# Kernel optimization log

Hardware: AMD Instinct MI355X
Metric: run time of the kernel (lower is better)

Reference implementation:

```python
import jax, jax.numpy as jnp
import numpy as np

N_NODES = 50000
N_EDGES = 800000
NUM_GRAPHS = 256
F_IN = 64        # num_features (per-head out dim == in dim in this module)
HEADS = 4        # n_heads1
OUT_DIM = 128    # output_dim
HC = HEADS * F_IN
NEG_SLOPE = 0.2  # GATConv leaky_relu slope
EPS = 1e-5       # GraphNorm eps


def setup_inputs() -> dict:
    key = jax.random.key(0)
    ks = jax.random.split(key, 12)
    s = lambda k, shape, fan: (jax.random.normal(k, shape, jnp.float32) / np.sqrt(fan).astype(np.float32))
    return {
        "x": jax.random.normal(ks[0], (N_NODES, F_IN), jnp.float32),
        "edge_index": jax.random.randint(ks[1], (2, N_EDGES), 0, N_NODES),
        "batch": jnp.sort(jax.random.randint(ks[2], (N_NODES,), 0, NUM_GRAPHS)),
        # GATConv params
        "lin_w": s(ks[3], (HC, F_IN), F_IN),
        "att_src": s(ks[4], (HEADS, F_IN), F_IN),
        "att_dst": s(ks[5], (HEADS, F_IN), F_IN),
        "gat_bias": jnp.zeros((HC,), jnp.float32),
        # GraphNorm params
        "gn_weight": jnp.ones((HC,), jnp.float32),
        "gn_bias": jnp.zeros((HC,), jnp.float32),
        "gn_mean_scale": jnp.ones((HC,), jnp.float32),
        # fc_g1 / out heads
        "fc1_w": s(ks[6], (OUT_DIM, HC), HC), "fc1_b": jnp.zeros((OUT_DIM,), jnp.float32),
        "out_w": s(ks[7], (1, OUT_DIM), OUT_DIM), "out_b": jnp.zeros((1,), jnp.float32),
        # GlobalAttention gate_nn: Linear(HC,16) -> ReLU -> Linear(16,1) -> Sigmoid
        "att1_w": s(ks[8], (16, HC), HC), "att1_b": jnp.zeros((16,), jnp.float32),
        "att2_w": s(ks[9], (1, 16), 16), "att2_b": jnp.zeros((1,), jnp.float32),
    }


def _gat_conv(x, edge_index, lin_w, att_src, att_dst, gat_bias):
    """PyG GATConv with add_self_loops=True, concat heads. Returns (out [N,HC], alpha [E+N,H])."""
    N = x.shape[0]
    xh = (x @ lin_w.T).reshape(N, HEADS, F_IN)                 # [N,H,C]
    a_src = (xh * att_src[None]).sum(-1)                        # [N,H]
    a_dst = (xh * att_dst[None]).sum(-1)                        # [N,H]
    loops = jnp.arange(N)
    src = jnp.concatenate([edge_index[0], loops])               # [E+N]
    dst = jnp.concatenate([edge_index[1], loops])
    alpha = jax.nn.leaky_relu(a_src[src] + a_dst[dst], NEG_SLOPE)  # [E+N,H]
    # segment softmax over incoming edges of each dst node (self-loops guarantee non-empty)
    amax = jax.ops.segment_max(alpha, dst, num_segments=N)
    alpha = jnp.exp(alpha - amax[dst])
    denom = jax.ops.segment_sum(alpha, dst, num_segments=N)
    alpha = alpha / (denom[dst] + 1e-16)
    msg = xh[src] * alpha[:, :, None]                           # [E+N,H,C]
    out = jax.ops.segment_sum(msg, dst, num_segments=N).reshape(N, HC) + gat_bias
    return out, alpha


def _graph_norm(x, batch, weight, bias, mean_scale):
    ones = jnp.ones((x.shape[0],), x.dtype)
    cnt = jnp.maximum(jax.ops.segment_sum(ones, batch, num_segments=NUM_GRAPHS), 1.0)[:, None]
    mean = jax.ops.segment_sum(x, batch, num_segments=NUM_GRAPHS) / cnt
    sub = x - mean[batch] * mean_scale
    var = jax.ops.segment_sum(sub * sub, batch, num_segments=NUM_GRAPHS) / cnt
    return weight * sub / jnp.sqrt(var + EPS)[batch] + bias


def _global_attention(x, batch, att1_w, att1_b, att2_w, att2_b):
    gate = jax.nn.sigmoid(jax.nn.relu(x @ att1_w.T + att1_b) @ att2_w.T + att2_b)  # [N,1]
    gmax = jax.ops.segment_max(gate, batch, num_segments=NUM_GRAPHS)
    gate = jnp.exp(gate - gmax[batch])
    gden = jax.ops.segment_sum(gate, batch, num_segments=NUM_GRAPHS)
    gate = gate / (gden[batch] + 1e-16)
    return jax.ops.segment_sum(gate * x, batch, num_segments=NUM_GRAPHS)  # [G,HC]


def reference(x, edge_index, batch, lin_w, att_src, att_dst, gat_bias,
              gn_weight, gn_bias, gn_mean_scale, fc1_w, fc1_b, out_w, out_b,
              att1_w, att1_b, att2_w, att2_b):
    x2, alpha = _gat_conv(x, edge_index, lin_w, att_src, att_dst, gat_bias)
    h = _graph_norm(x2, batch, gn_weight, gn_bias, gn_mean_scale)
    h = jax.nn.relu(h)                                # node_dropout = identity (eval)
    pooled = _global_attention(h, batch, att1_w, att1_b, att2_w, att2_b)
    h = jax.nn.relu(pooled @ fc1_w.T + fc1_b)          # dropout = identity (eval)
    out = jax.nn.sigmoid(h @ out_w.T + out_b)          # [G,1]
    return out, alpha
```

## Files before the change

kernel.cpp:

```cpp
#include <hip/hip_runtime.h>
#include <hip/hip_fp16.h>
#include <math.h>

#define NN 50000
#define NE 800000
#define NG 256
#define NEG_SLOPE 0.2f
#define GEPS 1e-5f
#define CHUNK 64
#define NB 196
#define CAP 6144
#define EPB 3125
#define SPLIT 8
#define NLINB 782
#define ABLK 3321

typedef _Float16 f16x8 __attribute__((ext_vector_type(8)));
typedef _Float16 f16x4 __attribute__((ext_vector_type(4)));
typedef float f32x4 __attribute__((ext_vector_type(4)));
typedef float f32x2 __attribute__((ext_vector_type(2)));

__device__ __forceinline__ float lrelu(float v){ return v > 0.f ? v : NEG_SLOPE * v; }

__global__ __launch_bounds__(256) void k_misc(const float* __restrict__ lin_w,
                                              _Float16* __restrict__ wh,
                                              const float* __restrict__ att1_w,
                                              _Float16* __restrict__ a1w,
                                              const int* __restrict__ batch,
                                              int* __restrict__ goff,
                                              int* __restrict__ gcnt,
                                              int* __restrict__ bucket_cnt) {
  int b = blockIdx.x, tid = threadIdx.x;
  if (b == 0) {
    if (tid < NB) bucket_cnt[tid] = 0;
    int g = tid;
    int lo = 0, hi = NN;
    while (lo < hi) { int mid = (lo + hi) >> 1; if (batch[mid] < g) lo = mid + 1; else hi = mid; }
    int start = lo;
    lo = 0; hi = NN;
    while (lo < hi) { int mid = (lo + hi) >> 1; if (batch[mid] < g + 1) lo = mid + 1; else hi = mid; }
    goff[g] = start;
    gcnt[g] = lo - start;
  } else if (b <= 16) {
    int i0 = (b - 1) * 1024 + tid * 4;
    float4 f = *(const float4*)&lin_w[i0];
    f16x4 h4;
    h4[0] = (_Float16)f.x; h4[1] = (_Float16)f.y; h4[2] = (_Float16)f.z; h4[3] = (_Float16)f.w;
    *(f16x4*)&wh[i0] = h4;
  } else {
    int i0 = (b - 17) * 1024 + tid * 4;
    float4 f = *(const float4*)&att1_w[i0];
    f16x4 h4;
    h4[0] = (_Float16)f.x; h4[1] = (_Float16)f.y; h4[2] = (_Float16)f.z; h4[3] = (_Float16)f.w;
    *(f16x4*)&a1w[i0] = h4;
  }
}

__device__ __forceinline__ void lin_body(char* smem,
                                         const float* __restrict__ x,
                                         const _Float16* __restrict__ wh,
                                         const float* __restrict__ att_src,
                                         const float* __restrict__ att_dst,
                                         unsigned char* __restrict__ xh8,
                                         float* __restrict__ a_src_n,
                                         float* __restrict__ a_dst_n) {
  unsigned char* s_f8 = (unsigned char*)smem;
  int w = threadIdx.x >> 6, lane = threadIdx.x & 63;
  int nb = blockIdx.x * 64 + w * 16;
  if (nb >= NN) return;
  int am = lane & 15, quad = lane >> 4;
  int wb = w * 4096;

  const float* xr = x + (size_t)(nb + am) * 64 + quad * 8;
  float4 f0 = *(const float4*)(xr);
  float4 f1 = *(const float4*)(xr + 4);
  float4 f2 = *(const float4*)(xr + 32);
  float4 f3 = *(const float4*)(xr + 36);
  f16x8 a0, a1;
  a0[0] = (_Float16)f0.x; a0[1] = (_Float16)f0.y; a0[2] = (_Float16)f0.z; a0[3] = (_Float16)f0.w;
  a0[4] = (_Float16)f1.x; a0[5] = (_Float16)f1.y; a0[6] = (_Float16)f1.z; a0[7] = (_Float16)f1.w;
  a1[0] = (_Float16)f2.x; a1[1] = (_Float16)f2.y; a1[2] = (_Float16)f2.z; a1[3] = (_Float16)f2.w;
  a1[4] = (_Float16)f3.x; a1[5] = (_Float16)f3.y; a1[6] = (_Float16)f3.z; a1[7] = (_Float16)f3.w;

  f32x4 acc[16];
#pragma unroll
  for (int ct = 0; ct < 16; ct++) acc[ct] = (f32x4){0.f, 0.f, 0.f, 0.f};

#pragma unroll
  for (int ct = 0; ct < 16; ct++) {
    const _Float16* wbp = wh + (size_t)(ct * 16 + am) * 64 + quad * 8;
    f16x8 b0 = *(const f16x8*)(wbp);
    f16x8 b1 = *(const f16x8*)(wbp + 32);
    acc[ct] = __builtin_amdgcn_mfma_f32_16x16x32_f16(a0, b0, acc[ct], 0, 0, 0);
    acc[ct] = __builtin_amdgcn_mfma_f32_16x16x32_f16(a1, b1, acc[ct], 0, 0, 0);
  }

  float ps[4][4], pd[4][4];
#pragma unroll
  for (int r = 0; r < 4; r++)
#pragma unroll
    for (int h = 0; h < 4; h++) { ps[r][h] = 0.f; pd[r][h] = 0.f; }
#pragma unroll
  for (int ct = 0; ct < 16; ct++) {
    int c = ct * 16 + am;
    float av = att_src[c];
    float dv = att_dst[c];
    int h = ct >> 2;
#pragma unroll
    for (int r = 0; r < 4; r++) {
      float v = acc[ct][r];
      ps[r][h] += v * av;
      pd[r][h] += v * dv;
    }
  }
#pragma unroll
  for (int r = 0; r < 4; r++)
#pragma unroll
    for (int h = 0; h < 4; h++) {
      float s = ps[r][h], d = pd[r][h];
#pragma unroll
      for (int o = 1; o < 16; o <<= 1) {
        s += __shfl_xor(s, o, 64);
        d += __shfl_xor(d, o, 64);
      }
      if (am == 0) {
        int node = nb + quad * 4 + r;
        a_src_n[node * 4 + h] = s;
        a_dst_n[node * 4 + h] = d;
      }
    }

#pragma unroll
  for (int r = 0; r < 4; r++) {
    uint4 u;
    int t;
    t = __builtin_amdgcn_cvt_pk_fp8_f32(acc[0][r],  acc[1][r],  0, 0);
    t = __builtin_amdgcn_cvt_pk_fp8_f32(acc[2][r],  acc[3][r],  t, 1);
    u.x = (unsigned)t;
    t = __builtin_amdgcn_cvt_pk_fp8_f32(acc[4][r],  acc[5][r],  0, 0);
    t = __builtin_amdgcn_cvt_pk_fp8_f32(acc[6][r],  acc[7][r],  t, 1);
    u.y = (unsigned)t;
    t = __builtin_amdgcn_cvt_pk_fp8_f32(acc[8][r],  acc[9][r],  0, 0);
    t = __builtin_amdgcn_cvt_pk_fp8_f32(acc[10][r], acc[11][r], t, 1);
    u.z = (unsigned)t;
    t = __builtin_amdgcn_cvt_pk_fp8_f32(acc[12][r], acc[13][r], 0, 0);
    t = __builtin_amdgcn_cvt_pk_fp8_f32(acc[14][r], acc[15][r], t, 1);
    u.w = (unsigned)t;
    *(uint4*)&s_f8[wb + (quad * 4 + r) * 256 + am * 16] = u;
  }
#pragma unroll
  for (int p = 0; p < 4; p++) {
    uint4 u = *(const uint4*)&s_f8[wb + p * 1024 + lane * 16];
    *(uint4*)&xh8[(size_t)nb * 256 + p * 1024 + lane * 16] = u;
  }
}

__device__ __forceinline__ void binA_body(char* smem, int b,
                                          const int* __restrict__ ei,
                                          int* __restrict__ bucket_cnt,
                                          int2* __restrict__ ebuf) {
  int2* sorted = (int2*)smem;
  int*  hist   = (int*)(smem + 25024);
  int*  lbase  = (int*)(smem + 25824);
  int*  cur    = (int*)(smem + 26624);
  int*  runb   = (int*)(smem + 27424);
  int*  wsum   = (int*)(smem + 28224);
  int tid = threadIdx.x, lane = tid & 63, wid = tid >> 6;
  int e0 = b * EPB, e1 = min(e0 + EPB, NE);
  int n = e1 - e0;
  for (int i = tid; i < NB; i += 256) hist[i] = 0;
  __syncthreads();
  for (int e = e0 + tid; e < e1; e += 256) atomicAdd(&hist[ei[NE + e] >> 8], 1);
  __syncthreads();
  {
    int v = (tid < NB) ? hist[tid] : 0;
    int s = v;
#pragma unroll
    for (int o = 1; o < 64; o <<= 1) { int t = __shfl_up(s, o, 64); if (lane >= o) s += t; }
    if (lane == 63) wsum[wid] = s;
    __syncthreads();
    int wbase = 0;
    for (int k = 0; k < wid; k++) wbase += wsum[k];
    if (tid < NB) {
      int ex = wbase + s - v;
      lbase[tid] = ex;
      cur[tid] = ex;
      runb[tid] = atomicAdd(&bucket_cnt[tid], v);
    }
  }
  __syncthreads();
  for (int e = e0 + tid; e < e1; e += 256) {
    int d = ei[NE + e], s = ei[e];
    int lp = atomicAdd(&cur[d >> 8], 1);
    sorted[lp] = make_int2(d, s);
  }
  __syncthreads();
  for (int i = tid; i < n; i += 256) {
    int2 e = sorted[i];
    int bk = e.x >> 8;
    int slot = runb[bk] + (i - lbase[bk]);
    if (slot < CAP) ebuf[(size_t)bk * CAP + slot] = e;
  }
}

__global__ __launch_bounds__(256) void k_linbin(const float* __restrict__ x,
                                                const _Float16* __restrict__ wh,
                                                const float* __restrict__ att_src,
                                                const float* __restrict__ att_dst,
                                                unsigned char* __restrict__ xh8,
                                                float* __restrict__ a_src_n,
                                                float* __restrict__ a_dst_n,
                                                const int* __restrict__ ei,
                                                int* __restrict__ bucket_cnt,
                                                int2* __restrict__ ebuf) {
  __shared__ __align__(16) char smem[28240];
  if (blockIdx.x < NLINB)
    lin_body(smem, x, wh, att_src, att_dst, xh8, a_src_n, a_dst_n);
  else
    binA_body(smem, blockIdx.x - NLINB, ei, bucket_cnt, ebuf);
}

__global__ __launch_bounds__(256) void k_binB(const int2* __restrict__ ebuf,
                                              const int* __restrict__ bucket_cnt,
                                              int* __restrict__ deg,
                                              int* __restrict__ offs,
                                              int* __restrict__ src_list) {
  __shared__ int hist[256];
  __shared__ int cur[256];
  __shared__ int wsum[4];
  __shared__ int bbase[NB];
  int b = blockIdx.x, tid = threadIdx.x, lane = tid & 63, wid = tid >> 6;
  {
    int v = (tid < NB) ? min(bucket_cnt[tid], CAP) : 0;
    int s = v;
#pragma unroll
    for (int o = 1; o < 64; o <<= 1) { int t = __shfl_up(s, o, 64); if (lane >= o) s += t; }
    if (lane == 63) wsum[wid] = s;
    __syncthreads();
    int wbase = 0;
    for (int k = 0; k < wid; k++) wbase += wsum[k];
    if (tid < NB) bbase[tid] = wbase + s - v;
  }
  __syncthreads();
  int cnt = min(bucket_cnt[b], CAP);
  int base = bbase[b];
  const int2* seg = ebuf + (size_t)b * CAP;
  hist[tid] = 0;
  __syncthreads();
  for (int i = tid; i < cnt; i += 256) atomicAdd(&hist[seg[i].x & 255], 1);
  __syncthreads();
  int v = hist[tid];
  int s = v;
#pragma unroll
  for (int o = 1; o < 64; o <<= 1) { int t = __shfl_up(s, o, 64); if (lane >= o) s += t; }
  if (lane == 63) wsum[wid] = s;
  __syncthreads();
  int wbase = 0;
  for (int k = 0; k < wid; k++) wbase += wsum[k];
  int excl = wbase + s - v;
  int node = b * 256 + tid;
  if (node < NN) {
    deg[node] = v;
    offs[node] = base + excl;
  }
  cur[tid] = excl;
  __syncthreads();
  for (int i = tid; i < cnt; i += 256) {
    int2 e = seg[i];
    int pos = base + atomicAdd(&cur[e.x & 255], 1);
    src_list[pos] = e.y;
  }
}

__global__ __launch_bounds__(64) void k_gat(const unsigned char* __restrict__ xh8,
                                            const float* __restrict__ a_src_n,
                                            const float* __restrict__ a_dst_n,
                                            const int* __restrict__ offs,
                                            const int* __restrict__ deg_arr,
                                            const int* __restrict__ src_list,
                                            const float* __restrict__ gat_bias,
                                            __half* __restrict__ x2h,
                                            float* __restrict__ den_inv) {
  __shared__ __align__(16) float s_al[CHUNK * 4];
  __shared__ int s_src[CHUNK];
  __shared__ __half s_tr[256];
  int n = blockIdx.x, lane = threadIdx.x;
  int off = offs[n], dg = deg_arr[n], cnt = dg + 1;
  float4 ad = *(const float4*)&a_dst_n[n * 4];
  int h = lane & 3;
  unsigned loff = 4u * (unsigned)lane;
  float acc0 = 0.f, acc1 = 0.f, acc2 = 0.f, acc3 = 0.f;

  if (cnt <= 64) {
    float e0 = 0.f, e1 = 0.f, e2 = 0.f, e3 = 0.f;
    if (lane < cnt) {
      int src = (lane < dg) ? src_list[off + lane] : n;
      float4 as = *(const float4*)&a_src_n[src * 4];
      e0 = __expf(lrelu(as.x + ad.x));
      e1 = __expf(lrelu(as.y + ad.y));
      e2 = __expf(lrelu(as.z + ad.z));
      e3 = __expf(lrelu(as.w + ad.w));
      s_src[lane] = src;
    }
    float s0 = e0, s1 = e1, s2 = e2, s3 = e3;
#pragma unroll
    for (int o = 32; o >= 1; o >>= 1) {
      s0 += __shfl_xor(s0, o, 64);
      s1 += __shfl_xor(s1, o, 64);
      s2 += __shfl_xor(s2, o, 64);
      s3 += __shfl_xor(s3, o, 64);
    }
    float i0 = 1.f / (s0 + 1e-16f), i1 = 1.f / (s1 + 1e-16f);
    float i2 = 1.f / (s2 + 1e-16f), i3 = 1.f / (s3 + 1e-16f);
    if (lane == 0) *(float4*)&den_inv[n * 4] = make_float4(i0, i1, i2, i3);
    if (lane < cnt) {
      s_al[lane * 4 + 0] = e0 * i0;
      s_al[lane * 4 + 1] = e1 * i1;
      s_al[lane * 4 + 2] = e2 * i2;
      s_al[lane * 4 + 3] = e3 * i3;
    }
    __syncthreads();
    int j = 0;
    for (; j + 4 <= cnt; j += 4) {
      unsigned oA = ((unsigned)s_src[j] << 8) + loff;
      unsigned oB = ((unsigned)s_src[j + 1] << 8) + loff;
      unsigned oC = ((unsigned)s_src[j + 2] << 8) + loff;
      unsigned oD = ((unsigned)s_src[j + 3] << 8) + loff;
      unsigned rA = *(const unsigned*)&xh8[oA];
      unsigned rB = *(const unsigned*)&xh8[oB];
      unsigned rC = *(const unsigned*)&xh8[oC];
      unsigned rD = *(const unsigned*)&xh8[oD];
      float aA = s_al[j * 4 + h], aB = s_al[(j + 1) * 4 + h];
      float aC = s_al[(j + 2) * 4 + h], aD = s_al[(j + 3) * 4 + h];
      f32x2 lA = __builtin_amdgcn_cvt_pk_f32_fp8((int)rA, 0);
      f32x2 hA = __builtin_amdgcn_cvt_pk_f32_fp8((int)rA, 1);
      f32x2 lB = __builtin_amdgcn_cvt_pk_f32_fp8((int)rB, 0);
      f32x2 hB = __builtin_amdgcn_cvt_pk_f32_fp8((int)rB, 1);
      f32x2 lC = __builtin_amdgcn_cvt_pk_f32_fp8((int)rC, 0);
      f32x2 hC = __builtin_amdgcn_cvt_pk_f32_fp8((int)rC, 1);
      f32x2 lD = __builtin_amdgcn_cvt_pk_f32_fp8((int)rD, 0);
      f32x2 hD = __builtin_amdgcn_cvt_pk_f32_fp8((int)rD, 1);
      acc0 += aA * lA[0] + aB * lB[0] + aC * lC[0] + aD * lD[0];
      acc1 += aA * lA[1] + aB * lB[1] + aC * lC[1] + aD * lD[1];
      acc2 += aA * hA[0] + aB * hB[0] + aC * hC[0] + aD * hD[0];
      acc3 += aA * hA[1] + aB * hB[1] + aC * hC[1] + aD * hD[1];
    }
    for (; j < cnt; j++) {
      unsigned oA = ((unsigned)s_src[j] << 8) + loff;
      unsigned rA = *(const unsigned*)&xh8[oA];
      float aA = s_al[j * 4 + h];
      f32x2 lA = __builtin_amdgcn_cvt_pk_f32_fp8((int)rA, 0);
      f32x2 hA = __builtin_amdgcn_cvt_pk_f32_fp8((int)rA, 1);
      acc0 += aA * lA[0];
      acc1 += aA * lA[1];
      acc2 += aA * hA[0];
      acc3 += aA * hA[1];
    }
  } else {
    float s0 = 0.f, s1 = 0.f, s2 = 0.f, s3 = 0.f;
    for (int j = lane; j < cnt; j += 64) {
      int src = (j < dg) ? src_list[off + j] : n;
      float4 as = *(const float4*)&a_src_n[src * 4];
      s0 += __expf(lrelu(as.x + ad.x));
      s1 += __expf(lrelu(as.y + ad.y));
      s2 += __expf(lrelu(as.z + ad.z));
      s3 += __expf(lrelu(as.w + ad.w));
    }
#pragma unroll
    for (int o = 32; o >= 1; o >>= 1) {
      s0 += __shfl_xor(s0, o, 64);
      s1 += __shfl_xor(s1, o, 64);
      s2 += __shfl_xor(s2, o, 64);
      s3 += __shfl_xor(s3, o, 64);
    }
    float i0 = 1.f / (s0 + 1e-16f), i1 = 1.f / (s1 + 1e-16f);
    float i2 = 1.f / (s2 + 1e-16f), i3 = 1.f / (s3 + 1e-16f);
    if (lane == 0) *(float4*)&den_inv[n * 4] = make_float4(i0, i1, i2, i3);
    for (int cb = 0; cb < cnt; cb += CHUNK) {
      int clen = min(CHUNK, cnt - cb);
      for (int j = lane; j < clen; j += 64) {
        int jj = cb + j;
        int src = (jj < dg) ? src_list[off + jj] : n;
        float4 as = *(const float4*)&a_src_n[src * 4];
        s_src[j] = src;
        s_al[j * 4 + 0] = __expf(lrelu(as.x + ad.x)) * i0;
        s_al[j * 4 + 1] = __expf(lrelu(as.y + ad.y)) * i1;
        s_al[j * 4 + 2] = __expf(lrelu(as.z + ad.z)) * i2;
        s_al[j * 4 + 3] = __expf(lrelu(as.w + ad.w)) * i3;
      }
      __syncthreads();
      for (int j = 0; j < clen; j++) {
        unsigned oA = ((unsigned)s_src[j] << 8) + loff;
        unsigned rA = *(const unsigned*)&xh8[oA];
        float aA = s_al[j * 4 + h];
        f32x2 lA = __builtin_amdgcn_cvt_pk_f32_fp8((int)rA, 0);
        f32x2 hA = __builtin_amdgcn_cvt_pk_f32_fp8((int)rA, 1);
        acc0 += aA * lA[0];
        acc1 += aA * lA[1];
        acc2 += aA * hA[0];
        acc3 += aA * hA[1];
      }
      __syncthreads();
    }
  }

  int cb0 = (lane & 3) * 64 + (lane >> 2);
  s_tr[cb0 +  0] = __float2half(acc0 + gat_bias[cb0 +  0]);
  s_tr[cb0 + 16] = __float2half(acc1 + gat_bias[cb0 + 16]);
  s_tr[cb0 + 32] = __float2half(acc2 + gat_bias[cb0 + 32]);
  s_tr[cb0 + 48] = __float2half(acc3 + gat_bias[cb0 + 48]);
  __syncthreads();
  uint2 u = *(const uint2*)&s_tr[4 * lane];
  *(uint2*)&x2h[(size_t)n * 256 + 4 * lane] = u;
}

__global__ __launch_bounds__(256) void k_alst(const int* __restrict__ ei,
                                              const float* __restrict__ a_src_n,
                                              const float* __restrict__ a_dst_n,
                                              const float* __restrict__ den_inv,
                                              float* __restrict__ alpha_out,
                                              const __half* __restrict__ x2h,
                                              const int* __restrict__ gcnt,
                                              const int* __restrict__ goff,
                                              float* __restrict__ psumA,
                                              float* __restrict__ psumB) {
  if (blockIdx.x < ABLK) {
    int idx = blockIdx.x * 256 + threadIdx.x;
    if (idx >= NE + NN) return;
    int s, d;
    if (idx < NE) { s = ei[idx]; d = ei[NE + idx]; }
    else          { s = idx - NE; d = s; }
    float4 as = *(const float4*)&a_src_n[s * 4];
    float4 ad = *(const float4*)&a_dst_n[d * 4];
    float4 iv = *(const float4*)&den_inv[d * 4];
    float4 a;
    a.x = __expf(lrelu(as.x + ad.x)) * iv.x;
    a.y = __expf(lrelu(as.y + ad.y)) * iv.y;
    a.z = __expf(lrelu(as.z + ad.z)) * iv.z;
    a.w = __expf(lrelu(as.w + ad.w)) * iv.w;
    *(float4*)&alpha_out[(size_t)idx * 4] = a;
  } else {
    int b = blockIdx.x - ABLK, c = threadIdx.x;
    int g = b >> 3, s = b & 7;
    int cnt = gcnt[g], start = goff[g];
    const __half* p = x2h + (size_t)start * 256 + c;
    float sum = 0.f, sum2 = 0.f;
    int i = s;
    for (; i + 56 < cnt; i += 64) {
      float v0 = __half2float(p[(size_t)(i +  0) * 256]);
      float v1 = __half2float(p[(size_t)(i +  8) * 256]);
      float v2 = __half2float(p[(size_t)(i + 16) * 256]);
      float v3 = __half2float(p[(size_t)(i + 24) * 256]);
      float v4 = __half2float(p[(size_t)(i + 32) * 256]);
      float v5 = __half2float(p[(size_t)(i + 40) * 256]);
      float v6 = __half2float(p[(size_t)(i + 48) * 256]);
      float v7 = __half2float(p[(size_t)(i + 56) * 256]);
      sum += ((v0 + v1) + (v2 + v3)) + ((v4 + v5) + (v6 + v7));
      sum2 += ((v0 * v0 + v1 * v1) + (v2 * v2 + v3 * v3)) +
              ((v4 * v4 + v5 * v5) + (v6 * v6 + v7 * v7));
    }
    for (; i < cnt; i += 8) { float v = __half2float(p[(size_t)i * 256]); sum += v; sum2 += v * v; }
    psumA[b * 256 + c] = sum;
    psumB[b * 256 + c] = sum2;
  }
}

__global__ __launch_bounds__(256) void k_stats2(const float* __restrict__ psumA,
                                                const float* __restrict__ psumB,
                                                const int* __restrict__ gcnt,
                                                const float* __restrict__ gn_w,
                                                const float* __restrict__ gn_b,
                                                const float* __restrict__ gn_ms,
                                                float* __restrict__ scale_g,
                                                float* __restrict__ shift_g) {
  int g = blockIdx.x, c = threadIdx.x;
  int b0 = g * SPLIT;
  float S = 0.f, S2 = 0.f;
#pragma unroll
  for (int k = 0; k < SPLIT; k++) {
    S  += psumA[(b0 + k) * 256 + c];
    S2 += psumB[(b0 + k) * 256 + c];
  }
  float fc = fmaxf((float)gcnt[g], 1.f);
  float mean = S / fc;
  float mm = mean * gn_ms[c];
  float var = fmaxf(S2 / fc - 2.f * mm * mean + mm * mm, 0.f);
  float sc = gn_w[c] / sqrtf(var + GEPS);
  scale_g[g * 256 + c] = sc;
  shift_g[g * 256 + c] = gn_b[c] - sc * mm;
}

__global__ __launch_bounds__(256) void k_gate(const __half* __restrict__ x2h,
                                              const int* __restrict__ batch,
                                              const float* __restrict__ scale_g,
                                              const float* __restrict__ shift_g,
                                              const _Float16* __restrict__ a1w,
                                              const float* __restrict__ att1_b,
                                              const float* __restrict__ att2_w,
                                              const float* __restrict__ att2_b,
                                              float* __restrict__ gate_raw) {
  int w = threadIdx.x >> 6, lane = threadIdx.x & 63;
  int nb = blockIdx.x * 64 + w * 16;
  if (nb >= NN) return;
  int am = lane & 15, quad = lane >> 4;
  int node = nb + am;
  int g = batch[node];

  const __half*   xp  = x2h + (size_t)node * 256 + quad * 8;
  const float*    scp = scale_g + g * 256 + quad * 8;
  const float*    shp = shift_g + g * 256 + quad * 8;
  const _Float16* bp  = a1w + am * 256 + quad * 8;

  f32x4 acc = (f32x4){0.f, 0.f, 0.f, 0.f};
#pragma unroll
  for (int kb = 0; kb < 8; kb++) {
    f16x8 xv = *(const f16x8*)(xp + kb * 32);
    float4 sc0 = *(const float4*)(scp + kb * 32);
    float4 sc1 = *(const float4*)(scp + kb * 32 + 4);
    float4 sh0 = *(const float4*)(shp + kb * 32);
    float4 sh1 = *(const float4*)(shp + kb * 32 + 4);
    f16x8 a;
    a[0] = (_Float16)fmaxf(sc0.x * (float)xv[0] + sh0.x, 0.f);
    a[1] = (_Float16)fmaxf(sc0.y * (float)xv[1] + sh0.y, 0.f);
    a[2] = (_Float16)fmaxf(sc0.z * (float)xv[2] + sh0.z, 0.f);
    a[3] = (_Float16)fmaxf(sc0.w * (float)xv[3] + sh0.w, 0.f);
    a[4] = (_Float16)fmaxf(sc1.x * (float)xv[4] + sh1.x, 0.f);
    a[5] = (_Float16)fmaxf(sc1.y * (float)xv[5] + sh1.y, 0.f);
    a[6] = (_Float16)fmaxf(sc1.z * (float)xv[6] + sh1.z, 0.f);
    a[7] = (_Float16)fmaxf(sc1.w * (float)xv[7] + sh1.w, 0.f);
    f16x8 b = *(const f16x8*)(bp + kb * 32);
    acc = __builtin_amdgcn_mfma_f32_16x16x32_f16(a, b, acc, 0, 0, 0);
  }

  float b1 = att1_b[am], w2 = att2_w[am], b2 = att2_b[0];
#pragma unroll
  for (int r = 0; r < 4; r++) {
    float t = w2 * fmaxf(acc[r] + b1, 0.f);
#pragma unroll
    for (int o = 1; o < 16; o <<= 1) t += __shfl_xor(t, o, 64);
    if (am == 0) gate_raw[nb + quad * 4 + r] = 1.f / (1.f + __expf(-(t + b2)));
  }
}

__global__ __launch_bounds__(256) void k_poolp(const __half* __restrict__ x2h,
                                               const float* __restrict__ gate_raw,
                                               const int* __restrict__ gcnt,
                                               const int* __restrict__ goff,
                                               const float* __restrict__ scale_g,
                                               const float* __restrict__ shift_g,
                                               float* __restrict__ ppool) {
  __shared__ float s_w[1024];
  __shared__ float red[4];
  int b = blockIdx.x, c = threadIdx.x, lane = c & 63, wid = c >> 6;
  int g = b >> 3, s = b & 7;
  int cnt = gcnt[g], start = goff[g];
  float ls = 0.f;
  for (int i = c; i < cnt; i += 256) {
    float e = __expf(gate_raw[start + i]);
    s_w[i] = e;
    ls += e;
  }
#pragma unroll
  for (int o = 32; o >= 1; o >>= 1) ls += __shfl_xor(ls, o, 64);
  if (lane == 0) red[wid] = ls;
  __syncthreads();
  float rden = 1.f / (red[0] + red[1] + red[2] + red[3] + 1e-16f);

  float sc = scale_g[g * 256 + c], sh = shift_g[g * 256 + c];
  const __half* p = x2h + (size_t)start * 256 + c;
  float pooled = 0.f;
  int i = s;
  for (; i + 56 < cnt; i += 64) {
    float v0 = __half2float(p[(size_t)(i +  0) * 256]);
    float v1 = __half2float(p[(size_t)(i +  8) * 256]);
    float v2 = __half2float(p[(size_t)(i + 16) * 256]);
    float v3 = __half2float(p[(size_t)(i + 24) * 256]);
    float v4 = __half2float(p[(size_t)(i + 32) * 256]);
    float v5 = __half2float(p[(size_t)(i + 40) * 256]);
    float v6 = __half2float(p[(size_t)(i + 48) * 256]);
    float v7 = __half2float(p[(size_t)(i + 56) * 256]);
    pooled += s_w[i +  0] * fmaxf(sc * v0 + sh, 0.f);
    pooled += s_w[i +  8] * fmaxf(sc * v1 + sh, 0.f);
    pooled += s_w[i + 16] * fmaxf(sc * v2 + sh, 0.f);
    pooled += s_w[i + 24] * fmaxf(sc * v3 + sh, 0.f);
    pooled += s_w[i + 32] * fmaxf(sc * v4 + sh, 0.f);
    pooled += s_w[i + 40] * fmaxf(sc * v5 + sh, 0.f);
    pooled += s_w[i + 48] * fmaxf(sc * v6 + sh, 0.f);
    pooled += s_w[i + 56] * fmaxf(sc * v7 + sh, 0.f);
  }
  for (; i < cnt; i += 8)
    pooled += s_w[i] * fmaxf(sc * __half2float(p[(size_t)i * 256]) + sh, 0.f);
  ppool[b * 256 + c] = pooled * rden;
}

__global__ __launch_bounds__(256) void k_fin(const float* __restrict__ ppool,
                                             const float* __restrict__ fc1_w,
                                             const float* __restrict__ fc1_b,
                                             const float* __restrict__ out_w,
                                             const float* __restrict__ out_b,
                                             float* __restrict__ outp) {
  __shared__ __align__(16) float pool_s[256];
  __shared__ float hred[128];
  __shared__ float red[4];
  int g = blockIdx.x, tid = threadIdx.x, lane = tid & 63, wid = tid >> 6;
  int b0 = g * SPLIT;
  float acc = 0.f;
#pragma unroll
  for (int k = 0; k < SPLIT; k++) acc += ppool[(b0 + k) * 256 + tid];
  pool_s[tid] = acc;
  __syncthreads();
  float4 psv = *(const float4*)&pool_s[4 * lane];
  for (int j0 = 0; j0 < 32; j0++) {
    int j = wid * 32 + j0;
    float4 w = *(const float4*)&fc1_w[j * 256 + 4 * lane];
    float d = w.x * psv.x + w.y * psv.y + w.z * psv.z + w.w * psv.w;
#pragma unroll
    for (int o = 32; o >= 1; o >>= 1) d += __shfl_xor(d, o, 64);
    if (lane == 0) hred[j] = fmaxf(d + fc1_b[j], 0.f) * out_w[j];
  }
  __syncthreads();
  if (tid < 128) {
    float v = hred[tid];
#pragma unroll
    for (int o = 32; o >= 1; o >>= 1) v += __shfl_xor(v, o, 64);
    if (lane == 0) red[wid] = v;
  }
  __syncthreads();
  if (tid == 0) outp[g] = 1.f / (1.f + __expf(-(red[0] + red[1] + out_b[0])));
}

extern "C" void kernel_launch(void* const* d_in, const int* in_sizes, int n_in,
                              void* d_out, int out_size, void* d_ws, size_t ws_size,
                              hipStream_t stream) {
  const float* x        = (const float*)d_in[0];
  const int*   ei       = (const int*)d_in[1];
  const int*   batch    = (const int*)d_in[2];
  const float* lin_w    = (const float*)d_in[3];
  const float* att_src  = (const float*)d_in[4];
  const float* att_dst  = (const float*)d_in[5];
  const float* gat_bias = (const float*)d_in[6];
  const float* gn_w     = (const float*)d_in[7];
  const float* gn_b     = (const float*)d_in[8];
  const float* gn_ms    = (const float*)d_in[9];
  const float* fc1_w    = (const float*)d_in[10];
  const float* fc1_b    = (const float*)d_in[11];
  const float* out_w    = (const float*)d_in[12];
  const float* out_b    = (const float*)d_in[13];
  const float* att1_w   = (const float*)d_in[14];
  const float* att1_b   = (const float*)d_in[15];
  const float* att2_w   = (const float*)d_in[16];
  const float* att2_b   = (const float*)d_in[17];

  float* outp  = (float*)d_out;
  float* alpha = outp + NG;

  char* wsb = (char*)d_ws;
  size_t o = 0;
  auto A = [&](size_t bytes) -> char* {
    char* p = wsb + o;
    o += (bytes + 255) & ~(size_t)255;
    return p;
  };
  unsigned char* xh8 = (unsigned char*)A((size_t)NN * 256);
  __half*   x2h      = (__half*)A((size_t)NN * 256 * 2);
  _Float16* wh       = (_Float16*)A((size_t)256 * 64 * 2);
  _Float16* a1w      = (_Float16*)A((size_t)16 * 256 * 2);
  float* a_src_n  = (float*)A((size_t)NN * 4 * 4);
  float* a_dst_n  = (float*)A((size_t)NN * 4 * 4);
  float* den_inv  = (float*)A((size_t)NN * 4 * 4);
  float* gate_raw = (float*)A((size_t)NN * 4);
  float* psumA    = (float*)A((size_t)NG * SPLIT * 256 * 4);
  float* psumB    = (float*)A((size_t)NG * SPLIT * 256 * 4);
  float* ppool    = (float*)A((size_t)NG * SPLIT * 256 * 4);
  float* scale_g  = (float*)A((size_t)NG * 256 * 4);
  float* shift_g  = (float*)A((size_t)NG * 256 * 4);
  int*   deg      = (int*)A((size_t)NN * 4);
  int*   gcnt     = (int*)A((size_t)NG * 4);
  int*   offs     = (int*)A((size_t)NN * 4);
  int*   goff     = (int*)A((size_t)NG * 4);
  int*   src_list = (int*)A((size_t)NE * 4);
  int2*  ebuf     = (int2*)A((size_t)NB * CAP * 8);
  int*   bucket_cnt  = (int*)A((size_t)NB * 4);

  k_misc<<<21, 256, 0, stream>>>(lin_w, wh, att1_w, a1w, batch, goff, gcnt, bucket_cnt);
  k_linbin<<<NLINB + 256, 256, 0, stream>>>(x, wh, att_src, att_dst, xh8, a_src_n, a_dst_n,
                                            ei, bucket_cnt, ebuf);
  k_binB<<<NB, 256, 0, stream>>>(ebuf, bucket_cnt, deg, offs, src_list);
  k_gat<<<NN, 64, 0, stream>>>(xh8, a_src_n, a_dst_n, offs, deg, src_list,
                               gat_bias, x2h, den_inv);
  k_alst<<<ABLK + NG * SPLIT, 256, 0, stream>>>(ei, a_src_n, a_dst_n, den_inv, alpha,
                                                x2h, gcnt, goff, psumA, psumB);
  k_stats2<<<NG, 256, 0, stream>>>(psumA, psumB, gcnt, gn_w, gn_b, gn_ms, scale_g, shift_g);
  k_gate<<<(NN + 63) / 64, 256, 0, stream>>>(x2h, batch, scale_g, shift_g, a1w, att1_b,
                                             att2_w, att2_b, gate_raw);
  k_poolp<<<NG * SPLIT, 256, 0, stream>>>(x2h, gate_raw, gcnt, goff, scale_g, shift_g, ppool);
  k_fin<<<NG, 256, 0, stream>>>(ppool, fc1_w, fc1_b, out_w, out_b, outp);
}
```

Baseline: 253.0 us.

## Fuse GraphNorm stats, gate, pooling and final MLP into one per-graph kernel

```diff
diff --git a/kernel.cpp b/kernel.cpp
--- a/kernel.cpp
+++ b/kernel.cpp
@@ -14,6 +14,7 @@
 #define SPLIT 8
 #define NLINB 782
 #define ABLK 3321
+#define GMAX 512
 
 typedef _Float16 f16x8 __attribute__((ext_vector_type(8)));
 typedef _Float16 f16x4 __attribute__((ext_vector_type(4)));
@@ -465,150 +466,131 @@
   }
 }
 
-__global__ __launch_bounds__(256) void k_stats2(const float* __restrict__ psumA,
-                                                const float* __restrict__ psumB,
-                                                const int* __restrict__ gcnt,
-                                                const float* __restrict__ gn_w,
-                                                const float* __restrict__ gn_b,
-                                                const float* __restrict__ gn_ms,
-                                                float* __restrict__ scale_g,
-                                                float* __restrict__ shift_g) {
-  int g = blockIdx.x, c = threadIdx.x;
-  int b0 = g * SPLIT;
-  float S = 0.f, S2 = 0.f;
-#pragma unroll
-  for (int k = 0; k < SPLIT; k++) {
-    S  += psumA[(b0 + k) * 256 + c];
-    S2 += psumB[(b0 + k) * 256 + c];
-  }
-  float fc = fmaxf((float)gcnt[g], 1.f);
-  float mean = S / fc;
-  float mm = mean * gn_ms[c];
-  float var = fmaxf(S2 / fc - 2.f * mm * mean + mm * mm, 0.f);
-  float sc = gn_w[c] / sqrtf(var + GEPS);
-  scale_g[g * 256 + c] = sc;
-  shift_g[g * 256 + c] = gn_b[c] - sc * mm;
-}
-
-__global__ __launch_bounds__(256) void k_gate(const __half* __restrict__ x2h,
-                                              const int* __restrict__ batch,
-                                              const float* __restrict__ scale_g,
-                                              const float* __restrict__ shift_g,
+__global__ __launch_bounds__(256) void k_tail(const float* __restrict__ psumA,
+                                              const float* __restrict__ psumB,
+                                              const int* __restrict__ gcnt,
+                                              const int* __restrict__ goff,
+                                              const float* __restrict__ gn_w,
+                                              const float* __restrict__ gn_b,
+                                              const float* __restrict__ gn_ms,
+                                              const __half* __restrict__ x2h,
                                               const _Float16* __restrict__ a1w,
                                               const float* __restrict__ att1_b,
                                               const float* __restrict__ att2_w,
                                               const float* __restrict__ att2_b,
-                                              float* __restrict__ gate_raw) {
-  int w = threadIdx.x >> 6, lane = threadIdx.x & 63;
-  int nb = blockIdx.x * 64 + w * 16;
-  if (nb >= NN) return;
-  int am = lane & 15, quad = lane >> 4;
-  int node = nb + am;
-  int g = batch[node];
-
-  const __half*   xp  = x2h + (size_t)node * 256 + quad * 8;
-  const float*    scp = scale_g + g * 256 + quad * 8;
-  const float*    shp = shift_g + g * 256 + quad * 8;
-  const _Float16* bp  = a1w + am * 256 + quad * 8;
-
-  f32x4 acc = (f32x4){0.f, 0.f, 0.f, 0.f};
-#pragma unroll
-  for (int kb = 0; kb < 8; kb++) {
-    f16x8 xv = *(const f16x8*)(xp + kb * 32);
-    float4 sc0 = *(const float4*)(scp + kb * 32);
-    float4 sc1 = *(const float4*)(scp + kb * 32 + 4);
-    float4 sh0 = *(const float4*)(shp + kb * 32);
-    float4 sh1 = *(const float4*)(shp + kb * 32 + 4);
-    f16x8 a;
-    a[0] = (_Float16)fmaxf(sc0.x * (float)xv[0] + sh0.x, 0.f);
-    a[1] = (_Float16)fmaxf(sc0.y * (float)xv[1] + sh0.y, 0.f);
-    a[2] = (_Float16)fmaxf(sc0.z * (float)xv[2] + sh0.z, 0.f);
-    a[3] = (_Float16)fmaxf(sc0.w * (float)xv[3] + sh0.w, 0.f);
-    a[4] = (_Float16)fmaxf(sc1.x * (float)xv[4] + sh1.x, 0.f);
-    a[5] = (_Float16)fmaxf(sc1.y * (float)xv[5] + sh1.y, 0.f);
-    a[6] = (_Float16)fmaxf(sc1.z * (float)xv[6] + sh1.z, 0.f);
-    a[7] = (_Float16)fmaxf(sc1.w * (float)xv[7] + sh1.w, 0.f);
-    f16x8 b = *(const f16x8*)(bp + kb * 32);
-    acc = __builtin_amdgcn_mfma_f32_16x16x32_f16(a, b, acc, 0, 0, 0);
-  }
-
-  float b1 = att1_b[am], w2 = att2_w[am], b2 = att2_b[0];
-#pragma unroll
-  for (int r = 0; r < 4; r++) {
-    float t = w2 * fmaxf(acc[r] + b1, 0.f);
-#pragma unroll
-    for (int o = 1; o < 16; o <<= 1) t += __shfl_xor(t, o, 64);
-    if (am == 0) gate_raw[nb + quad * 4 + r] = 1.f / (1.f + __expf(-(t + b2)));
-  }
-}
-
-__global__ __launch_bounds__(256) void k_poolp(const __half* __restrict__ x2h,
-                                               const float* __restrict__ gate_raw,
-                                               const int* __restrict__ gcnt,
-                                               const int* __restrict__ goff,
-                                               const float* __restrict__ scale_g,
-                                               const float* __restrict__ shift_g,
-                                               float* __restrict__ ppool) {
-  __shared__ float s_w[1024];
-  __shared__ float red[4];
-  int b = blockIdx.x, c = threadIdx.x, lane = c & 63, wid = c >> 6;
-  int g = b >> 3, s = b & 7;
-  int cnt = gcnt[g], start = goff[g];
-  float ls = 0.f;
-  for (int i = c; i < cnt; i += 256) {
-    float e = __expf(gate_raw[start + i]);
-    s_w[i] = e;
-    ls += e;
-  }
-#pragma unroll
-  for (int o = 32; o >= 1; o >>= 1) ls += __shfl_xor(ls, o, 64);
-  if (lane == 0) red[wid] = ls;
-  __syncthreads();
-  float rden = 1.f / (red[0] + red[1] + red[2] + red[3] + 1e-16f);
-
-  float sc = scale_g[g * 256 + c], sh = shift_g[g * 256 + c];
-  const __half* p = x2h + (size_t)start * 256 + c;
-  float pooled = 0.f;
-  int i = s;
-  for (; i + 56 < cnt; i += 64) {
-    float v0 = __half2float(p[(size_t)(i +  0) * 256]);
-    float v1 = __half2float(p[(size_t)(i +  8) * 256]);
-    float v2 = __half2float(p[(size_t)(i + 16) * 256]);
-    float v3 = __half2float(p[(size_t)(i + 24) * 256]);
-    float v4 = __half2float(p[(size_t)(i + 32) * 256]);
-    float v5 = __half2float(p[(size_t)(i + 40) * 256]);
-    float v6 = __half2float(p[(size_t)(i + 48) * 256]);
-    float v7 = __half2float(p[(size_t)(i + 56) * 256]);
-    pooled += s_w[i +  0] * fmaxf(sc * v0 + sh, 0.f);
-    pooled += s_w[i +  8] * fmaxf(sc * v1 + sh, 0.f);
-    pooled += s_w[i + 16] * fmaxf(sc * v2 + sh, 0.f);
-    pooled += s_w[i + 24] * fmaxf(sc * v3 + sh, 0.f);
-    pooled += s_w[i + 32] * fmaxf(sc * v4 + sh, 0.f);
-    pooled += s_w[i + 40] * fmaxf(sc * v5 + sh, 0.f);
-    pooled += s_w[i + 48] * fmaxf(sc * v6 + sh, 0.f);
-    pooled += s_w[i + 56] * fmaxf(sc * v7 + sh, 0.f);
-  }
-  for (; i < cnt; i += 8)
-    pooled += s_w[i] * fmaxf(sc * __half2float(p[(size_t)i * 256]) + sh, 0.f);
-  ppool[b * 256 + c] = pooled * rden;
-}
-
-__global__ __launch_bounds__(256) void k_fin(const float* __restrict__ ppool,
-                                             const float* __restrict__ fc1_w,
-                                             const float* __restrict__ fc1_b,
-                                             const float* __restrict__ out_w,
-                                             const float* __restrict__ out_b,
-                                             float* __restrict__ outp) {
+                                              const float* __restrict__ fc1_w,
+                                              const float* __restrict__ fc1_b,
+                                              const float* __restrict__ out_w,
+                                              const float* __restrict__ out_b,
+                                              float* __restrict__ outp) {
+  __shared__ __align__(16) float s_sc[256];
+  __shared__ __align__(16) float s_sh[256];
+  __shared__ float s_gate[GMAX];
   __shared__ __align__(16) float pool_s[256];
   __shared__ float hred[128];
   __shared__ float red[4];
   int g = blockIdx.x, tid = threadIdx.x, lane = tid & 63, wid = tid >> 6;
-  int b0 = g * SPLIT;
-  float acc = 0.f;
-#pragma unroll
-  for (int k = 0; k < SPLIT; k++) acc += ppool[(b0 + k) * 256 + tid];
-  pool_s[tid] = acc;
-  __syncthreads();
+  int cnt = gcnt[g], start = goff[g];
+
+  {
+    int b0 = g * SPLIT, c = tid;
+    float S = 0.f, S2 = 0.f;
+#pragma unroll
+    for (int k = 0; k < SPLIT; k++) {
+      S  += psumA[(b0 + k) * 256 + c];
+      S2 += psumB[(b0 + k) * 256 + c];
+    }
+    float fc = fmaxf((float)cnt, 1.f);
+    float mean = S / fc;
+    float mm = mean * gn_ms[c];
+    float var = fmaxf(S2 / fc - 2.f * mm * mean + mm * mm, 0.f);
+    float sc = gn_w[c] / sqrtf(var + GEPS);
+    s_sc[c] = sc;
+    s_sh[c] = gn_b[c] - sc * mm;
+  }
+  __syncthreads();
+
+  int am = lane & 15, quad = lane >> 4;
+  float b1 = att1_b[am], w2 = att2_w[am], b2 = att2_b[0];
+  const _Float16* bp = a1w + am * 256 + quad * 8;
+  for (int i0 = wid * 16; i0 < cnt; i0 += 64) {
+    int node = start + i0 + am;
+    if (node > NN - 1) node = NN - 1;
+    const __half* xp = x2h + (size_t)node * 256 + quad * 8;
+    f32x4 ga = (f32x4){0.f, 0.f, 0.f, 0.f};
+#pragma unroll
+    for (int kb = 0; kb < 8; kb++) {
+      f16x8 xv = *(const f16x8*)(xp + kb * 32);
+      int cb = quad * 8 + kb * 32;
+      float4 sc0 = *(const float4*)&s_sc[cb];
+      float4 sc1 = *(const float4*)&s_sc[cb + 4];
+      float4 sh0 = *(const float4*)&s_sh[cb];
+      float4 sh1 = *(const float4*)&s_sh[cb + 4];
+      f16x8 a;
+      a[0] = (_Float16)fmaxf(sc0.x * (float)xv[0] + sh0.x, 0.f);
+      a[1] = (_Float16)fmaxf(sc0.y * (float)xv[1] + sh0.y, 0.f);
+      a[2] = (_Float16)fmaxf(sc0.z * (float)xv[2] + sh0.z, 0.f);
+      a[3] = (_Float16)fmaxf(sc0.w * (float)xv[3] + sh0.w, 0.f);
+      a[4] = (_Float16)fmaxf(sc1.x * (float)xv[4] + sh1.x, 0.f);
+      a[5] = (_Float16)fmaxf(sc1.y * (float)xv[5] + sh1.y, 0.f);
+      a[6] = (_Float16)fmaxf(sc1.z * (float)xv[6] + sh1.z, 0.f);
+      a[7] = (_Float16)fmaxf(sc1.w * (float)xv[7] + sh1.w, 0.f);
+      f16x8 b = *(const f16x8*)(bp + kb * 32);
+      ga = __builtin_amdgcn_mfma_f32_16x16x32_f16(a, b, ga, 0, 0, 0);
+    }
+#pragma unroll
+    for (int r = 0; r < 4; r++) {
+      float t = w2 * fmaxf(ga[r] + b1, 0.f);
+#pragma unroll
+      for (int o = 1; o < 16; o <<= 1) t += __shfl_xor(t, o, 64);
+      if (am == 0) {
+        int li = i0 + quad * 4 + r;
+        if (li < cnt && li < GMAX)
+          s_gate[li] = __expf(1.f / (1.f + __expf(-(t + b2))));
+      }
+    }
+  }
+  __syncthreads();
+
+  float ls = 0.f;
+  for (int i = tid; i < cnt; i += 256) ls += s_gate[i];
+#pragma unroll
+  for (int o = 32; o >= 1; o >>= 1) ls += __shfl_xor(ls, o, 64);
+  if (lane == 0) red[wid] = ls;
+  __syncthreads();
+  float rden = 1.f / (red[0] + red[1] + red[2] + red[3] + 1e-16f);
+
+  {
+    int c = tid;
+    float sc = s_sc[c], sh = s_sh[c];
+    const __half* p = x2h + (size_t)start * 256 + c;
+    float a0 = 0.f, a1_ = 0.f, a2 = 0.f, a3 = 0.f;
+    float a4 = 0.f, a5 = 0.f, a6 = 0.f, a7 = 0.f;
+    int i = 0;
+    for (; i + 7 < cnt; i += 8) {
+      float v0 = __half2float(p[(size_t)(i + 0) * 256]);
+      float v1 = __half2float(p[(size_t)(i + 1) * 256]);
+      float v2 = __half2float(p[(size_t)(i + 2) * 256]);
+      float v3 = __half2float(p[(size_t)(i + 3) * 256]);
+      float v4 = __half2float(p[(size_t)(i + 4) * 256]);
+      float v5 = __half2float(p[(size_t)(i + 5) * 256]);
+      float v6 = __half2float(p[(size_t)(i + 6) * 256]);
+      float v7 = __half2float(p[(size_t)(i + 7) * 256]);
+      a0 += s_gate[i + 0] * fmaxf(sc * v0 + sh, 0.f);
+      a1_ += s_gate[i + 1] * fmaxf(sc * v1 + sh, 0.f);
+      a2 += s_gate[i + 2] * fmaxf(sc * v2 + sh, 0.f);
+      a3 += s_gate[i + 3] * fmaxf(sc * v3 + sh, 0.f);
+      a4 += s_gate[i + 4] * fmaxf(sc * v4 + sh, 0.f);
+      a5 += s_gate[i + 5] * fmaxf(sc * v5 + sh, 0.f);
+      a6 += s_gate[i + 6] * fmaxf(sc * v6 + sh, 0.f);
+      a7 += s_gate[i + 7] * fmaxf(sc * v7 + sh, 0.f);
+    }
+    for (; i < cnt; i++)
+      a0 += s_gate[i] * fmaxf(sc * __half2float(p[(size_t)i * 256]) + sh, 0.f);
+    pool_s[c] = ((((a0 + a1_) + (a2 + a3)) + ((a4 + a5) + (a6 + a7)))) * rden;
+  }
+  __syncthreads();
+
   float4 psv = *(const float4*)&pool_s[4 * lane];
   for (int j0 = 0; j0 < 32; j0++) {
     int j = wid * 32 + j0;
@@ -668,12 +650,8 @@
   float* a_src_n  = (float*)A((size_t)NN * 4 * 4);
   float* a_dst_n  = (float*)A((size_t)NN * 4 * 4);
   float* den_inv  = (float*)A((size_t)NN * 4 * 4);
-  float* gate_raw = (float*)A((size_t)NN * 4);
   float* psumA    = (float*)A((size_t)NG * SPLIT * 256 * 4);
   float* psumB    = (float*)A((size_t)NG * SPLIT * 256 * 4);
-  float* ppool    = (float*)A((size_t)NG * SPLIT * 256 * 4);
-  float* scale_g  = (float*)A((size_t)NG * 256 * 4);
-  float* shift_g  = (float*)A((size_t)NG * 256 * 4);
   int*   deg      = (int*)A((size_t)NN * 4);
   int*   gcnt     = (int*)A((size_t)NG * 4);
   int*   offs     = (int*)A((size_t)NN * 4);
@@ -690,9 +668,7 @@
                                gat_bias, x2h, den_inv);
   k_alst<<<ABLK + NG * SPLIT, 256, 0, stream>>>(ei, a_src_n, a_dst_n, den_inv, alpha,
                                                 x2h, gcnt, goff, psumA, psumB);
-  k_stats2<<<NG, 256, 0, stream>>>(psumA, psumB, gcnt, gn_w, gn_b, gn_ms, scale_g, shift_g);
-  k_gate<<<(NN + 63) / 64, 256, 0, stream>>>(x2h, batch, scale_g, shift_g, a1w, att1_b,
-                                             att2_w, att2_b, gate_raw);
-  k_poolp<<<NG * SPLIT, 256, 0, stream>>>(x2h, gate_raw, gcnt, goff, scale_g, shift_g, ppool);
-  k_fin<<<NG, 256, 0, stream>>>(ppool, fc1_w, fc1_b, out_w, out_b, outp);
-}
+  k_tail<<<NG, 256, 0, stream>>>(psumA, psumB, gcnt, goff, gn_w, gn_b, gn_ms, x2h,
+                                 a1w, att1_b, att2_w, att2_b, fc1_w, fc1_b,
+                                 out_w, out_b, outp);
+}
```

After: 233.9 us. 1.08x faster.
